# Kernel optimization log

Hardware: AMD Instinct MI355X
Metric: run time of the kernel (lower is better)

Reference implementation:

```python
import jax, jax.numpy as jnp
import numpy as np

B, D_IN = 4096, 1024
E, K = 16, 2
EMB = 256
H1, H2 = 2048, 1024  # hidden_units, hidden_units // 2
O = 512              # num_classes


def setup_inputs() -> dict:
    key = jax.random.key(0)
    ks = jax.random.split(key, 10)
    s = lambda *sh: 1.0 / np.sqrt(sh[-2] if len(sh) > 1 else 1.0)
    return {
        "x":   jax.random.normal(ks[0], (B, D_IN), jnp.float32),
        "Wr":  jax.random.normal(ks[1], (D_IN, EMB), jnp.float32) * (1.0 / np.sqrt(D_IN)),
        "br":  jnp.zeros((EMB,), jnp.float32),
        "emb": jax.random.normal(ks[2], (E, EMB), jnp.float32) * (1.0 / np.sqrt(EMB)),
        "W1":  jax.random.normal(ks[3], (E, D_IN, H1), jnp.float32) * (1.0 / np.sqrt(D_IN)),
        "b1":  jnp.zeros((E, H1), jnp.float32),
        "W2":  jax.random.normal(ks[4], (E, H1, H2), jnp.float32) * (1.0 / np.sqrt(H1)),
        "b2":  jnp.zeros((E, H2), jnp.float32),
        "W3":  jax.random.normal(ks[5], (E, H2, O), jnp.float32) * (1.0 / np.sqrt(H2)),
        "b3":  jnp.zeros((E, O), jnp.float32),
    }


def reference(x, Wr, br, emb, W1, b1, W2, b2, W3, b3):
    # Router query: [B, EMB]
    q = x @ Wr + br
    # Negative squared euclidean distance to expert embeddings -> scores [B, E]
    d2 = jnp.sum(jnp.square(q[:, None, :] - emb[None, :, :]), axis=-1)
    scores = -d2
    gating_probs = jax.nn.softmax(scores, axis=-1)  # [B, E]
    # Top-k selection + renormalized gates
    top_v, top_i = jax.lax.top_k(scores, K)          # [B, K]
    gates = jax.nn.softmax(top_v, axis=-1)           # [B, K]
    # All experts run on full batch (dense), batched over expert axis
    h1 = jax.nn.relu(jnp.einsum('bi,eih->beh', x, W1) + b1)   # [B, E, H1]
    h2 = jax.nn.relu(jnp.einsum('beh,ehm->bem', h1, W2) + b2)  # [B, E, H2]
    out = jnp.einsum('bem,emo->beo', h2, W3) + b3              # [B, E, O]
    # Gather top-k expert outputs per example and combine
    sel = jnp.take_along_axis(out, top_i[:, :, None], axis=1)  # [B, K, O]
    final = jnp.sum(sel * gates[:, :, None], axis=1)           # [B, O]
    return final, q, gating_probs
```

## Files before the change

### kernel.cpp

```cpp
#include <hip/hip_runtime.h>
#include <hip/hip_bf16.h>

using bf16 = __hip_bfloat16;
typedef __attribute__((ext_vector_type(8))) short bf16x8;
typedef __attribute__((ext_vector_type(8))) unsigned short u16x8;
typedef __attribute__((ext_vector_type(4))) float f32x4;

constexpr int BATCH = 4096;
constexpr int D_IN  = 1024;
constexpr int NEXP  = 16;
constexpr int EMB   = 256;
constexpr int H1    = 2048;
constexpr int H2    = 1024;
constexpr int OUTD  = 512;
constexpr int SLOTS = BATCH * 2;
constexpr int SLOTS_PAD = SLOTS + 256;
constexpr int MAX_T128 = SLOTS / 128 + NEXP;
constexpr int K3    = 3 * D_IN;

constexpr size_t WS_XB     = 0;
constexpr size_t WS_XLO    = WS_XB     + (size_t)BATCH * D_IN * 2;
constexpr size_t WS_H1     = WS_XLO    + (size_t)BATCH * D_IN * 2;
constexpr size_t WS_H2     = WS_H1     + (size_t)SLOTS_PAD * H1 * 2;
constexpr size_t WS_OSL    = WS_H2     + (size_t)SLOTS_PAD * H2 * 2;
constexpr size_t WS_TOPI   = WS_OSL    + (size_t)SLOTS_PAD * OUTD * 4;
constexpr size_t WS_GATES  = WS_TOPI   + (size_t)SLOTS * 4;
constexpr size_t WS_SLOTOF = WS_GATES  + (size_t)SLOTS * 4;
constexpr size_t WS_TOKL   = WS_SLOTOF + (size_t)SLOTS * 4;
constexpr size_t WS_CNT    = WS_TOKL   + (size_t)SLOTS_PAD * 4;
constexpr size_t WS_TMAP   = WS_CNT    + 64 * 4;
constexpr size_t WS_WR3    = ((WS_TMAP + (size_t)MAX_T128 * 8) + 255) & ~(size_t)255;
constexpr size_t WS_WT     = ((WS_WR3 + (size_t)EMB * K3 * 2) + 255) & ~(size_t)255;
constexpr size_t WT_BYTES  = (size_t)NEXP * H1 * D_IN * 2;
constexpr size_t WS_WTB    = WS_WT + WT_BYTES;
constexpr size_t WS_NEED_FUSED = WS_WTB + WT_BYTES;

__device__ __forceinline__ unsigned short f2bf(float f) {
    bf16 h = __float2bfloat16(f);
    return __builtin_bit_cast(unsigned short, h);
}
__device__ __forceinline__ float bf2f(unsigned short h) {
    return __builtin_bit_cast(float, (unsigned)h << 16);
}

__device__ __forceinline__ void gload16(const unsigned short* g, unsigned short* l) {
    __builtin_amdgcn_global_load_lds(
        (const __attribute__((address_space(1))) unsigned int*)g,
        (__attribute__((address_space(3))) unsigned int*)l, 16, 0, 0);
}

template <int N>
__device__ __forceinline__ void waitcnt_vm() {
    if constexpr (N == 0)       asm volatile("s_waitcnt vmcnt(0)" ::: "memory");
    else if constexpr (N == 4)  asm volatile("s_waitcnt vmcnt(4)" ::: "memory");
    else if constexpr (N == 6)  asm volatile("s_waitcnt vmcnt(6)" ::: "memory");
    else if constexpr (N == 8)  asm volatile("s_waitcnt vmcnt(8)" ::: "memory");
    else if constexpr (N == 12) asm volatile("s_waitcnt vmcnt(12)" ::: "memory");
    else static_assert(N == 0, "add case");
}

__device__ __forceinline__ void wtrans_body(const float* __restrict__ W,
                                            unsigned short* __restrict__ Wt,
                                            int KD, int ND, int e, int k0, int n0,
                                            char* smem) {
    float* Tf = (float*)smem;
    int t  = threadIdx.x;
    int kr = t >> 4, c4 = (t & 15) * 4;
    const float* Wb = W + ((size_t)e * KD + k0) * ND + n0;
#pragma unroll
    for (int i = 0; i < 4; i++) {
        float4 v = *reinterpret_cast<const float4*>(Wb + (size_t)(kr + i * 16) * ND + c4);
        Tf[(kr + i * 16) * 65 + c4 + 0] = v.x; Tf[(kr + i * 16) * 65 + c4 + 1] = v.y;
        Tf[(kr + i * 16) * 65 + c4 + 2] = v.z; Tf[(kr + i * 16) * 65 + c4 + 3] = v.w;
    }
    __syncthreads();
    unsigned short* Wtb = Wt + ((size_t)e * ND + n0) * KD + k0;
#pragma unroll
    for (int i = 0; i < 2; i++) {
        int idx = t + i * 256;
        int n = idx >> 3, ck = (idx & 7) * 8;
        u16x8 o;
#pragma unroll
        for (int j = 0; j < 8; j++) o[j] = f2bf(Tf[(ck + j) * 65 + n]);
        *reinterpret_cast<u16x8*>(Wtb + (size_t)n * KD + ck) = o;
    }
}

__global__ __launch_bounds__(256) void k_prep(const float* __restrict__ x,
                                              unsigned short* __restrict__ xhi,
                                              unsigned short* __restrict__ xlo,
                                              const float* __restrict__ Wr,
                                              unsigned short* __restrict__ Wrt3,
                                              int* __restrict__ counts) {
    __shared__ float Tf[64][65];
    int bx = blockIdx.x, t = threadIdx.x;
    if (bx < 4096) {
        int i = bx * 256 + t;
        float4 v = reinterpret_cast<const float4*>(x)[i];
        ushort4 h, l;
        h.x = f2bf(v.x); h.y = f2bf(v.y); h.z = f2bf(v.z); h.w = f2bf(v.w);
        l.x = f2bf(v.x - bf2f(h.x)); l.y = f2bf(v.y - bf2f(h.y));
        l.z = f2bf(v.z - bf2f(h.z)); l.w = f2bf(v.w - bf2f(h.w));
        reinterpret_cast<ushort4*>(xhi)[i] = h;
        reinterpret_cast<ushort4*>(xlo)[i] = l;
    } else if (bx < 4160) {
        int idx = bx - 4096;
        int n0 = (idx & 3) * 64, k0 = (idx >> 2) * 64;
        const float* Wb = Wr + (size_t)k0 * EMB + n0;
        int kr = t >> 4, c4 = (t & 15) * 4;
#pragma unroll
        for (int i = 0; i < 4; i++) {
            float4 v = *reinterpret_cast<const float4*>(Wb + (size_t)(kr + i * 16) * EMB + c4);
            Tf[kr + i * 16][c4 + 0] = v.x; Tf[kr + i * 16][c4 + 1] = v.y;
            Tf[kr + i * 16][c4 + 2] = v.z; Tf[kr + i * 16][c4 + 3] = v.w;
        }
        __syncthreads();
#pragma unroll
        for (int i = 0; i < 2; i++) {
            int idx2 = t + i * 256;
            int n = idx2 >> 3, ck = (idx2 & 7) * 8;
            u16x8 hi, lo;
#pragma unroll
            for (int j = 0; j < 8; j++) {
                float w = Tf[ck + j][n];
                unsigned short h = f2bf(w);
                hi[j] = h; lo[j] = f2bf(w - bf2f(h));
            }
            unsigned short* dst = Wrt3 + (size_t)(n0 + n) * K3 + k0 + ck;
            *reinterpret_cast<u16x8*>(dst)            = hi;
            *reinterpret_cast<u16x8*>(dst + D_IN)     = hi;
            *reinterpret_cast<u16x8*>(dst + 2 * D_IN) = lo;
        }
    } else {
        if (t < 16) counts[t] = 0;
    }
}

__global__ __launch_bounds__(256) void k_router_wt1(const unsigned short* __restrict__ xhi,
                                                    const unsigned short* __restrict__ xlo,
                                                    const unsigned short* __restrict__ wrt3,
                                                    const float* __restrict__ br,
                                                    float* __restrict__ qout,
                                                    const float* __restrict__ W1,
                                                    unsigned short* __restrict__ wt1) {
    __shared__ __align__(16) char smem[32768];
    int bx = blockIdx.x;
    if (bx >= 256) {
        int idx = bx - 256;
        int e   = idx >> 9;
        int rem = idx & 511;
        int k0  = (rem >> 5) << 6;
        int n0  = (rem & 31) << 6;
        wtrans_body(W1, wt1, D_IN, H1, e, k0, n0, smem);
        return;
    }
    unsigned short* As = (unsigned short*)smem;
    unsigned short* Bs = As + 8192;
    int nb = (bx & 3) * 64;
    int mb = (bx >> 2) * 64;

    int t    = threadIdx.x;
    int lane = t & 63;
    int w    = t >> 6;
    int wr   = (w >> 1) * 32;
    int wc   = (w & 1) * 32;

    int srow = t >> 3;
    int swz  = (t & 7) ^ (srow & 7);
    size_t aoff[2], boff[2];
#pragma unroll
    for (int i = 0; i < 2; i++) {
        int row = i * 32 + srow;
        aoff[i] = (size_t)(mb + row) * D_IN + swz * 8;
        boff[i] = (size_t)(nb + row) * K3 + swz * 8;
    }

    auto STAGE = [&](int buf, int tts) {
        const unsigned short* abase = (tts >= 16 && tts < 32) ? xlo : xhi;
        int kk = (tts & 15) * 64;
#pragma unroll
        for (int i = 0; i < 2; i++) {
            gload16(abase + aoff[i] + kk, As + buf * 4096 + (i * 32 + w * 8) * 64 + lane * 8);
            gload16(wrt3 + boff[i] + tts * 64, Bs + buf * 4096 + (i * 32 + w * 8) * 64 + lane * 8);
        }
    };

    f32x4 acc[2][2];
#pragma unroll
    for (int mi = 0; mi < 2; mi++)
#pragma unroll
        for (int ni = 0; ni < 2; ni++) acc[mi][ni] = {0.f, 0.f, 0.f, 0.f};

    int lr  = lane & 15;
    int lkc = lane >> 4;

    constexpr int NT = K3 / 64;
    STAGE(0, 0);
    STAGE(1, 1);

    for (int tt = 0; tt < NT; tt++) {
        int cur = tt & 1;
        if (tt + 1 < NT) waitcnt_vm<4>(); else waitcnt_vm<0>();
        __builtin_amdgcn_s_barrier();
        const char* Ab = (const char*)(As + cur * 4096);
        const char* Bb = (const char*)(Bs + cur * 4096);
#pragma unroll
        for (int ks = 0; ks < 2; ks++) {
            bf16x8 a[2], b[2];
#pragma unroll
            for (int mi = 0; mi < 2; mi++) {
                int row = wr + mi * 16 + lr;
                int c   = (lkc + ks * 4) ^ (row & 7);
                a[mi] = *reinterpret_cast<const bf16x8*>(Ab + row * 128 + c * 16);
            }
#pragma unroll
            for (int ni = 0; ni < 2; ni++) {
                int row = wc + ni * 16 + lr;
                int c   = (lkc + ks * 4) ^ (row & 7);
                b[ni] = *reinterpret_cast<const bf16x8*>(Bb + row * 128 + c * 16);
            }
#pragma unroll
            for (int mi = 0; mi < 2; mi++)
#pragma unroll
                for (int ni = 0; ni < 2; ni++)
                    acc[mi][ni] = __builtin_amdgcn_mfma_f32_16x16x32_bf16(a[mi], b[ni], acc[mi][ni], 0, 0, 0);
        }
        __builtin_amdgcn_s_barrier();
        if (tt + 2 < NT) STAGE(cur, tt + 2);
    }

    int rowbase = (lane >> 4) * 4;
#pragma unroll
    for (int ni = 0; ni < 2; ni++) {
        int col = nb + wc + ni * 16 + lr;
        float bv = br[col];
#pragma unroll
        for (int mi = 0; mi < 2; mi++) {
#pragma unroll
            for (int qi = 0; qi < 4; qi++) {
                int row = mb + wr + mi * 16 + rowbase + qi;
                qout[(size_t)row * EMB + col] = acc[mi][ni][qi] + bv;
            }
        }
    }
}

__global__ __launch_bounds__(256) void k_topk_count(const float* __restrict__ q,
                                                    const float* __restrict__ emb,
                                                    float* __restrict__ gp,
                                                    int* __restrict__ topi,
                                                    float* __restrict__ gates,
                                                    int* __restrict__ counts) {
    int b    = blockIdx.x * 4 + (threadIdx.x >> 6);
    int lane = threadIdx.x & 63;
    int e    = lane & 15;
    int seg  = (lane >> 4) * 64;
    const float* qr = q + (size_t)b * EMB + seg;
    const float* er = emb + (size_t)e * EMB + seg;
    float d2 = 0.f;
#pragma unroll 8
    for (int i = 0; i < 64; i++) { float d = qr[i] - er[i]; d2 = fmaf(d, d, d2); }
    d2 += __shfl_xor(d2, 16);
    d2 += __shfl_xor(d2, 32);
    float s = -d2;
    float m = s;
#pragma unroll
    for (int o = 1; o < 16; o <<= 1) m = fmaxf(m, __shfl_xor(m, o));
    float ex  = __expf(s - m);
    float sum = ex;
#pragma unroll
    for (int o = 1; o < 16; o <<= 1) sum += __shfl_xor(sum, o);
    if (lane < 16) gp[(size_t)b * NEXP + lane] = ex / sum;
    float v1 = s; int i1 = e;
#pragma unroll
    for (int o = 1; o < 16; o <<= 1) {
        float ov = __shfl_xor(v1, o); int oi = __shfl_xor(i1, o);
        if (ov > v1 || (ov == v1 && oi < i1)) { v1 = ov; i1 = oi; }
    }
    float s2 = (e == i1) ? -1e30f : s;
    float v2 = s2; int i2 = e;
#pragma unroll
    for (int o = 1; o < 16; o <<= 1) {
        float ov = __shfl_xor(v2, o); int oi = __shfl_xor(i2, o);
        if (ov > v2 || (ov == v2 && oi < i2)) { v2 = ov; i2 = oi; }
    }
    if (lane == 0) {
        topi[b * 2] = i1; topi[b * 2 + 1] = i2;
        float tv  = __expf(v2 - v1);
        float inv = 1.f / (1.f + tv);
        gates[b * 2] = inv; gates[b * 2 + 1] = tv * inv;
        atomicAdd(&counts[i1], 1);
        atomicAdd(&counts[i2], 1);
    }
}

__global__ void k_scan(const int* __restrict__ counts, int* __restrict__ offsets,
                       int* __restrict__ cursors, int2* __restrict__ tmap) {
    if (threadIdx.x != 0) return;
    int off = 0;
    for (int e = 0; e < NEXP; e++) {
        offsets[e] = off; cursors[e] = off;
        off += counts[e];
    }
    int nt = 0;
    for (int e = 0; e < NEXP; e++) {
        int c = counts[e];
        for (int base = 0; base < c; base += 128) tmap[nt++] = make_int2(e, base);
    }
    for (; nt < MAX_T128; nt++) tmap[nt] = make_int2(-1, 0);
}

__global__ __launch_bounds__(256) void k_scatter(const int* __restrict__ topi, int* __restrict__ cursors,
                                                 int* __restrict__ toklist, int* __restrict__ slotof) {
    int i = blockIdx.x * 256 + threadIdx.x;
    int e = topi[i];
    int s = atomicAdd(&cursors[e], 1);
    toklist[s] = i >> 1;
    slotof[i]  = s;
}

__global__ __launch_bounds__(256) void k_wtrans(const float* __restrict__ W,
                                                unsigned short* __restrict__ Wt,
                                                int KD, int ND) {
    __shared__ __align__(16) char smem[64 * 65 * 4];
    wtrans_body(W, Wt, KD, ND, blockIdx.z, blockIdx.y * 64, blockIdx.x * 64, smem);
}

template <int KD, int ND, int WN, int MODE, int KD2, int ND2, int DO_WT>
__global__ __launch_bounds__(WN * 64, 2) void k_gemm_wt(
    const unsigned short* __restrict__ Xin, const unsigned short* __restrict__ Wt,
    const float* __restrict__ bg, unsigned short* __restrict__ Hout,
    float* __restrict__ Oout, const int* __restrict__ counts,
    const int* __restrict__ offsets, const int* __restrict__ toklist,
    const int2* __restrict__ tmap, const float* __restrict__ Wnext,
    unsigned short* __restrict__ Wtnext) {
    constexpr int THREADS = WN * 64;
    constexpr int BM = 128;
    constexpr int BN = WN * 64;
    constexpr int FM = 8;
    constexpr int FN = 4;
    constexpr int RPI   = THREADS / 8;
    constexpr int A_ISS = (BM / 2) / RPI;
    constexpr int B_ISS = (BN / 2) / RPI;
    constexpr int SL    = A_ISS + B_ISS;
    constexpr int NX    = ND / BN;
    constexpr int NB_G  = NX * MAX_T128;
    constexpr int ABUF  = (BM / 2) * 64;
    constexpr int BBUF  = (BN / 2) * 64;

    __shared__ __align__(16) char smem[3 * (ABUF + BBUF) * 2];

    int bx = blockIdx.x;
    if (bx >= NB_G) {
        if constexpr (DO_WT) {
            constexpr int NBLK2 = ND2 / 64;
            constexpr int KBLK2 = KD2 / 64;
            int idx = bx - NB_G;
            int e   = idx / (NBLK2 * KBLK2);
            int rem = idx % (NBLK2 * KBLK2);
            int k0  = (rem / NBLK2) * 64;
            int n0  = (rem % NBLK2) * 64;
            wtrans_body(Wnext, Wtnext, KD2, ND2, e, k0, n0, smem);
        }
        return;
    }

    int2 tm = tmap[bx % MAX_T128];
    int e = tm.x;
    if (e < 0) return;
    int base = tm.y;
    int n_e  = counts[e];
    int off  = offsets[e];
    int n0   = (bx / MAX_T128) * BN;

    unsigned short* Asp = (unsigned short*)smem;
    unsigned short* Bsp = Asp + 3 * ABUF;

    int t    = threadIdx.x;
    int lane = t & 63;
    int w    = t >> 6;
    int wn   = w;

    int srow  = t >> 3;
    int chunk = t & 7;
    const unsigned short* asrc[A_ISS];
    const unsigned short* bsrc[B_ISS];
#pragma unroll
    for (int i = 0; i < A_ISS; i++) {
        int r  = i * RPI + srow;
        int js = chunk ^ (r & 7);
        int m_local = 2 * r + (js >> 2);
        int koff    = (js & 3) * 8;
        int g = base + m_local;
        size_t arow;
        if (MODE == 0) {
            int gg = (g < n_e) ? g : (n_e - 1);
            arow = (size_t)toklist[off + gg];
        } else {
            arow = (size_t)(off + g);
        }
        asrc[i] = Xin + arow * KD + koff;
    }
#pragma unroll
    for (int i = 0; i < B_ISS; i++) {
        int r  = i * RPI + srow;
        int js = chunk ^ (r & 7);
        int n_local = 2 * r + (js >> 2);
        int koff    = (js & 3) * 8;
        bsrc[i] = Wt + ((size_t)e * ND + n0 + n_local) * KD + koff;
    }

    auto STAGE = [&](int buf, int kt) {
#pragma unroll
        for (int i = 0; i < A_ISS; i++)
            gload16(asrc[i] + kt, Asp + buf * ABUF + (i * RPI + w * 8) * 64 + lane * 8);
#pragma unroll
        for (int i = 0; i < B_ISS; i++)
            gload16(bsrc[i] + kt, Bsp + buf * BBUF + (i * RPI + w * 8) * 64 + lane * 8);
    };

    f32x4 acc[FM][FN];
#pragma unroll
    for (int mi = 0; mi < FM; mi++)
#pragma unroll
        for (int ni = 0; ni < FN; ni++) acc[mi][ni] = {0.f, 0.f, 0.f, 0.f};

    int lr  = lane & 15;
    int lkc = lane >> 4;
    int jrd    = (((lr & 1) << 2) + lkc) ^ ((lr >> 1) & 7);
    int abase_ = (lr >> 1) * 128 + jrd * 16;
    int bbase_ = wn * 4096 + (lr >> 1) * 128 + jrd * 16;

    constexpr int NT = KD / 32;
    STAGE(0, 0);
    STAGE(1, 32);
    STAGE(2, 64);

    int cur = 0;
    for (int tt = 0; tt < NT; tt++) {
        if (tt + 2 < NT)      waitcnt_vm<2 * SL>();
        else if (tt + 1 < NT) waitcnt_vm<SL>();
        else                  waitcnt_vm<0>();
        __builtin_amdgcn_s_barrier();
        const char* Ab = (const char*)(Asp + cur * ABUF);
        const char* Bb = (const char*)(Bsp + cur * BBUF);
        bf16x8 a[FM], b[FN];
#pragma unroll
        for (int ni = 0; ni < FN; ni++)
            b[ni] = *reinterpret_cast<const bf16x8*>(Bb + bbase_ + ni * 1024);
#pragma unroll
        for (int mi = 0; mi < FM; mi++)
            a[mi] = *reinterpret_cast<const bf16x8*>(Ab + abase_ + mi * 1024);
#pragma unroll
        for (int mi = 0; mi < FM; mi++)
#pragma unroll
            for (int ni = 0; ni < FN; ni++)
                acc[mi][ni] = __builtin_amdgcn_mfma_f32_16x16x32_bf16(a[mi], b[ni], acc[mi][ni], 0, 0, 0);
        __builtin_amdgcn_s_barrier();
        if (tt + 3 < NT) STAGE(cur, (tt + 3) * 32);
        cur = (cur == 2) ? 0 : cur + 1;
    }

    int rowbase = (lane >> 4) * 4;
#pragma unroll
    for (int ni = 0; ni < FN; ni++) {
        int col = n0 + wn * 64 + ni * 16 + lr;
        float bv = bg[(size_t)e * ND + col];
#pragma unroll
        for (int mi = 0; mi < FM; mi++) {
#pragma unroll
            for (int qi = 0; qi < 4; qi++) {
                int g = base + mi * 16 + rowbase + qi;
                if (g < n_e) {
                    float v = acc[mi][ni][qi] + bv;
                    if (MODE == 2) {
                        Oout[(size_t)(off + g) * ND + col] = v;
                    } else {
                        v = fmaxf(v, 0.f);
                        Hout[(size_t)(off + g) * ND + col] = f2bf(v);
                    }
                }
            }
        }
    }
}

__global__ __launch_bounds__(128) void k_combine(const float* __restrict__ osl,
                                                 const float* __restrict__ gates,
                                                 const int* __restrict__ slotof,
                                                 float* __restrict__ outf) {
    int b = blockIdx.x;
    int j = threadIdx.x;
    int s0 = slotof[b * 2], s1 = slotof[b * 2 + 1];
    float g0 = gates[b * 2], g1 = gates[b * 2 + 1];
    float4 o0 = reinterpret_cast<const float4*>(osl + (size_t)s0 * OUTD)[j];
    float4 o1 = reinterpret_cast<const float4*>(osl + (size_t)s1 * OUTD)[j];
    float4 r;
    r.x = g0 * o0.x + g1 * o1.x;
    r.y = g0 * o0.y + g1 * o1.y;
    r.z = g0 * o0.z + g1 * o1.z;
    r.w = g0 * o0.w + g1 * o1.w;
    reinterpret_cast<float4*>(outf + (size_t)b * OUTD)[j] = r;
}

extern "C" void kernel_launch(void* const* d_in, const int* in_sizes, int n_in,
                              void* d_out, int out_size, void* d_ws, size_t ws_size,
                              hipStream_t stream) {
    const float* x   = (const float*)d_in[0];
    const float* Wr  = (const float*)d_in[1];
    const float* br  = (const float*)d_in[2];
    const float* emb = (const float*)d_in[3];
    const float* W1  = (const float*)d_in[4];
    const float* b1  = (const float*)d_in[5];
    const float* W2  = (const float*)d_in[6];
    const float* b2  = (const float*)d_in[7];
    const float* W3  = (const float*)d_in[8];
    const float* b3  = (const float*)d_in[9];

    float* out_final = (float*)d_out;
    float* out_q     = out_final + (size_t)BATCH * OUTD;
    float* out_gp    = out_q + (size_t)BATCH * EMB;

    char* ws = (char*)d_ws;
    unsigned short* xb  = (unsigned short*)(ws + WS_XB);
    unsigned short* xlo = (unsigned short*)(ws + WS_XLO);
    unsigned short* h1  = (unsigned short*)(ws + WS_H1);
    unsigned short* h2  = (unsigned short*)(ws + WS_H2);
    float* osl    = (float*)(ws + WS_OSL);
    int*   topi   = (int*)(ws + WS_TOPI);
    float* gates  = (float*)(ws + WS_GATES);
    int*   slotof = (int*)(ws + WS_SLOTOF);
    int*   toklist= (int*)(ws + WS_TOKL);
    int*   counts = (int*)(ws + WS_CNT);
    int*   offsets= counts + 16;
    int*   cursors= counts + 32;
    int2*  tmap   = (int2*)(ws + WS_TMAP);
    unsigned short* wrt3 = (unsigned short*)(ws + WS_WR3);
    unsigned short* wtA  = (unsigned short*)(ws + WS_WT);

    const bool fused = (ws_size >= WS_NEED_FUSED);
    unsigned short* wtB = fused ? (unsigned short*)(ws + WS_WTB) : wtA;

    k_prep<<<4161, 256, 0, stream>>>(x, xb, xlo, Wr, wrt3, counts);
    k_router_wt1<<<256 + 8192, 256, 0, stream>>>(xb, xlo, wrt3, br, out_q, W1, wtA);
    k_topk_count<<<BATCH / 4, 256, 0, stream>>>(out_q, emb, out_gp, topi, gates, counts);
    k_scan<<<1, 64, 0, stream>>>(counts, offsets, cursors, tmap);
    k_scatter<<<SLOTS / 256, 256, 0, stream>>>(topi, cursors, toklist, slotof);

    if (fused) {
        k_gemm_wt<D_IN, H1, 4, 0, H1, H2, 1><<<640 + 8192, 256, 0, stream>>>(
            xb, wtA, b1, h1, nullptr, counts, offsets, toklist, tmap, W2, wtB);
        k_gemm_wt<H1, H2, 4, 1, H2, OUTD, 1><<<320 + 2048, 256, 0, stream>>>(
            h1, wtB, b2, h2, nullptr, counts, offsets, toklist, tmap, W3, wtA);
        k_gemm_wt<H2, OUTD, 4, 2, 64, 64, 0><<<160, 256, 0, stream>>>(
            h2, wtA, b3, nullptr, osl, counts, offsets, toklist, tmap, nullptr, nullptr);
    } else {
        k_gemm_wt<D_IN, H1, 4, 0, 64, 64, 0><<<640, 256, 0, stream>>>(
            xb, wtA, b1, h1, nullptr, counts, offsets, toklist, tmap, nullptr, nullptr);
        k_wtrans<<<dim3(H2 / 64, H1 / 64, NEXP), 256, 0, stream>>>(W2, wtA, H1, H2);
        k_gemm_wt<H1, H2, 4, 1, 64, 64, 0><<<320, 256, 0, stream>>>(
            h1, wtA, b2, h2, nullptr, counts, offsets, toklist, tmap, nullptr, nullptr);
        k_wtrans<<<dim3(OUTD / 64, H2 / 64, NEXP), 256, 0, stream>>>(W3, wtA, H2, OUTD);
        k_gemm_wt<H2, OUTD, 4, 2, 64, 64, 0><<<160, 256, 0, stream>>>(
            h2, wtA, b3, nullptr, osl, counts, offsets, toklist, tmap, nullptr, nullptr);
    }

    k_combine<<<BATCH, 128, 0, stream>>>(osl, gates, slotof, out_final);
}
```

Before: 440.7 us.

## Move weight transposes earlier and bin expert tiles per XCD in grouped GEMMs

All three expert weight transposes (W1, W2, W3 to bf16) now run inside the router and top-k kernels instead of the GEMM kernels. Each GEMM kernel then only does matrix work, and the transposes overlap with the small router and top-k kernels. The scan kernel now bin-packs each expert's 128-row tiles into 8 bins of capacity 10, and the GEMM maps blockIdx so that each XCD handles one bin, aiming for L2 reuse of weight and activation tiles within an XCD. This needs more workspace (a third transpose buffer). The bin cap may drop tiles if the expert load is very skewed.

After: 458.1 us. +3.9%, slower.

```diff
diff --git a/kernel.cpp b/kernel.cpp
--- a/kernel.cpp
+++ b/kernel.cpp
@@ -16,6 +16,7 @@
 constexpr int SLOTS = BATCH * 2;
 constexpr int SLOTS_PAD = SLOTS + 256;
 constexpr int MAX_T128 = SLOTS / 128 + NEXP;
+constexpr int BIN_CAP  = 10;
 constexpr int K3    = 3 * D_IN;
 
 constexpr size_t WS_XB     = 0;
@@ -32,8 +33,11 @@
 constexpr size_t WS_WR3    = ((WS_TMAP + (size_t)MAX_T128 * 8) + 255) & ~(size_t)255;
 constexpr size_t WS_WT     = ((WS_WR3 + (size_t)EMB * K3 * 2) + 255) & ~(size_t)255;
 constexpr size_t WT_BYTES  = (size_t)NEXP * H1 * D_IN * 2;
-constexpr size_t WS_WTB    = WS_WT + WT_BYTES;
-constexpr size_t WS_NEED_FUSED = WS_WTB + WT_BYTES;
+constexpr size_t WT3_BYTES = (size_t)NEXP * H2 * OUTD * 2;
+constexpr size_t WS_WTB    = WS_WT  + WT_BYTES;
+constexpr size_t WS_WTC    = WS_WTB + WT_BYTES;
+constexpr size_t NEED2     = WS_WTC;
+constexpr size_t NEED1     = WS_WTC + WT3_BYTES;
 
 __device__ __forceinline__ unsigned short f2bf(float f) {
     bf16 h = __float2bfloat16(f);
@@ -54,7 +58,6 @@
     if constexpr (N == 0)       asm volatile("s_waitcnt vmcnt(0)" ::: "memory");
     else if constexpr (N == 4)  asm volatile("s_waitcnt vmcnt(4)" ::: "memory");
     else if constexpr (N == 6)  asm volatile("s_waitcnt vmcnt(6)" ::: "memory");
-    else if constexpr (N == 8)  asm volatile("s_waitcnt vmcnt(8)" ::: "memory");
     else if constexpr (N == 12) asm volatile("s_waitcnt vmcnt(12)" ::: "memory");
     else static_assert(N == 0, "add case");
 }
@@ -136,22 +139,27 @@
     }
 }
 
-__global__ __launch_bounds__(256) void k_router_wt1(const unsigned short* __restrict__ xhi,
-                                                    const unsigned short* __restrict__ xlo,
-                                                    const unsigned short* __restrict__ wrt3,
-                                                    const float* __restrict__ br,
-                                                    float* __restrict__ qout,
-                                                    const float* __restrict__ W1,
-                                                    unsigned short* __restrict__ wt1) {
+__global__ __launch_bounds__(256) void k_router_wt(const unsigned short* __restrict__ xhi,
+                                                   const unsigned short* __restrict__ xlo,
+                                                   const unsigned short* __restrict__ wrt3,
+                                                   const float* __restrict__ br,
+                                                   float* __restrict__ qout,
+                                                   const float* __restrict__ W1,
+                                                   unsigned short* __restrict__ wt1,
+                                                   const float* __restrict__ W2,
+                                                   unsigned short* __restrict__ wt2) {
     __shared__ __align__(16) char smem[32768];
     int bx = blockIdx.x;
     if (bx >= 256) {
         int idx = bx - 256;
-        int e   = idx >> 9;
-        int rem = idx & 511;
-        int k0  = (rem >> 5) << 6;
-        int n0  = (rem & 31) << 6;
-        wtrans_body(W1, wt1, D_IN, H1, e, k0, n0, smem);
+        if (idx < 8192) {
+            int e = idx >> 9, rem = idx & 511;
+            wtrans_body(W1, wt1, D_IN, H1, e, (rem >> 5) << 6, (rem & 31) << 6, smem);
+        } else {
+            int i2 = idx - 8192;
+            int e = i2 >> 9, rem = i2 & 511;
+            wtrans_body(W2, wt2, H1, H2, e, (rem >> 4) << 6, (rem & 15) << 6, smem);
+        }
         return;
     }
     unsigned short* As = (unsigned short*)smem;
@@ -245,13 +253,23 @@
     }
 }
 
-__global__ __launch_bounds__(256) void k_topk_count(const float* __restrict__ q,
-                                                    const float* __restrict__ emb,
-                                                    float* __restrict__ gp,
-                                                    int* __restrict__ topi,
-                                                    float* __restrict__ gates,
-                                                    int* __restrict__ counts) {
-    int b    = blockIdx.x * 4 + (threadIdx.x >> 6);
+__global__ __launch_bounds__(256) void k_topk_wt3(const float* __restrict__ q,
+                                                  const float* __restrict__ emb,
+                                                  float* __restrict__ gp,
+                                                  int* __restrict__ topi,
+                                                  float* __restrict__ gates,
+                                                  int* __restrict__ counts,
+                                                  const float* __restrict__ W3,
+                                                  unsigned short* __restrict__ wt3) {
+    __shared__ __align__(16) char smem[64 * 65 * 4];
+    int bx = blockIdx.x;
+    if (bx >= 1024) {
+        int idx = bx - 1024;
+        int e = idx >> 7, rem = idx & 127;
+        wtrans_body(W3, wt3, H2, OUTD, e, (rem >> 3) << 6, (rem & 7) << 6, smem);
+        return;
+    }
+    int b    = bx * 4 + (threadIdx.x >> 6);
     int lane = threadIdx.x & 63;
     int e    = lane & 15;
     int seg  = (lane >> 4) * 64;
@@ -298,16 +316,28 @@
                        int* __restrict__ cursors, int2* __restrict__ tmap) {
     if (threadIdx.x != 0) return;
     int off = 0;
+    int nt_e[NEXP];
     for (int e = 0; e < NEXP; e++) {
         offsets[e] = off; cursors[e] = off;
+        nt_e[e] = (counts[e] + 127) >> 7;
         off += counts[e];
     }
-    int nt = 0;
+    for (int i = 0; i < MAX_T128; i++) tmap[i] = make_int2(-1, 0);
+    int binload[8] = {0, 0, 0, 0, 0, 0, 0, 0};
     for (int e = 0; e < NEXP; e++) {
-        int c = counts[e];
-        for (int base = 0; base < c; base += 128) tmap[nt++] = make_int2(e, base);
-    }
-    for (; nt < MAX_T128; nt++) tmap[nt] = make_int2(-1, 0);
+        int rem = nt_e[e], ti = 0;
+        while (rem > 0) {
+            int b = 0;
+            for (int q2 = 1; q2 < 8; q2++)
+                if (binload[q2] < binload[b]) b = q2;
+            int space = BIN_CAP - binload[b];
+            if (space <= 0) break;
+            int take = (rem < space) ? rem : space;
+            for (int i = 0; i < take; i++)
+                tmap[b * BIN_CAP + binload[b] + i] = make_int2(e, (ti + i) * 128);
+            binload[b] += take; ti += take; rem -= take;
+        }
+    }
 }
 
 __global__ __launch_bounds__(256) void k_scatter(const int* __restrict__ topi, int* __restrict__ cursors,
@@ -326,14 +356,13 @@
     wtrans_body(W, Wt, KD, ND, blockIdx.z, blockIdx.y * 64, blockIdx.x * 64, smem);
 }
 
-template <int KD, int ND, int WN, int MODE, int KD2, int ND2, int DO_WT>
-__global__ __launch_bounds__(WN * 64, 2) void k_gemm_wt(
+template <int KD, int ND, int WN, int MODE>
+__global__ __launch_bounds__(WN * 64, 2) void k_gemm(
     const unsigned short* __restrict__ Xin, const unsigned short* __restrict__ Wt,
     const float* __restrict__ bg, unsigned short* __restrict__ Hout,
     float* __restrict__ Oout, const int* __restrict__ counts,
     const int* __restrict__ offsets, const int* __restrict__ toklist,
-    const int2* __restrict__ tmap, const float* __restrict__ Wnext,
-    unsigned short* __restrict__ Wtnext) {
+    const int2* __restrict__ tmap) {
     constexpr int THREADS = WN * 64;
     constexpr int BM = 128;
     constexpr int BN = WN * 64;
@@ -343,38 +372,23 @@
     constexpr int A_ISS = (BM / 2) / RPI;
     constexpr int B_ISS = (BN / 2) / RPI;
     constexpr int SL    = A_ISS + B_ISS;
-    constexpr int NX    = ND / BN;
-    constexpr int NB_G  = NX * MAX_T128;
-    constexpr int ABUF  = (BM / 2) * 64;
-    constexpr int BBUF  = (BN / 2) * 64;
-
-    __shared__ __align__(16) char smem[3 * (ABUF + BBUF) * 2];
-
-    int bx = blockIdx.x;
-    if (bx >= NB_G) {
-        if constexpr (DO_WT) {
-            constexpr int NBLK2 = ND2 / 64;
-            constexpr int KBLK2 = KD2 / 64;
-            int idx = bx - NB_G;
-            int e   = idx / (NBLK2 * KBLK2);
-            int rem = idx % (NBLK2 * KBLK2);
-            int k0  = (rem / NBLK2) * 64;
-            int n0  = (rem % NBLK2) * 64;
-            wtrans_body(Wnext, Wtnext, KD2, ND2, e, k0, n0, smem);
-        }
-        return;
-    }
-
-    int2 tm = tmap[bx % MAX_T128];
+
+    int id   = blockIdx.x;
+    int xcd  = id & 7;
+    int j    = id >> 3;
+    int y    = xcd * BIN_CAP + j % BIN_CAP;
+    int xnb  = j / BIN_CAP;
+
+    int2 tm = tmap[y];
     int e = tm.x;
     if (e < 0) return;
     int base = tm.y;
     int n_e  = counts[e];
     int off  = offsets[e];
-    int n0   = (bx / MAX_T128) * BN;
-
-    unsigned short* Asp = (unsigned short*)smem;
-    unsigned short* Bsp = Asp + 3 * ABUF;
+    int n0   = xnb * BN;
+
+    __shared__ __align__(16) unsigned short As[3][(BM / 2) * 64];
+    __shared__ __align__(16) unsigned short Bs[3][(BN / 2) * 64];
 
     int t    = threadIdx.x;
     int lane = t & 63;
@@ -413,10 +427,10 @@
     auto STAGE = [&](int buf, int kt) {
 #pragma unroll
         for (int i = 0; i < A_ISS; i++)
-            gload16(asrc[i] + kt, Asp + buf * ABUF + (i * RPI + w * 8) * 64 + lane * 8);
+            gload16(asrc[i] + kt, &As[buf][(i * RPI + w * 8) * 64] + lane * 8);
 #pragma unroll
         for (int i = 0; i < B_ISS; i++)
-            gload16(bsrc[i] + kt, Bsp + buf * BBUF + (i * RPI + w * 8) * 64 + lane * 8);
+            gload16(bsrc[i] + kt, &Bs[buf][(i * RPI + w * 8) * 64] + lane * 8);
     };
 
     f32x4 acc[FM][FN];
@@ -442,8 +456,8 @@
         else if (tt + 1 < NT) waitcnt_vm<SL>();
         else                  waitcnt_vm<0>();
         __builtin_amdgcn_s_barrier();
-        const char* Ab = (const char*)(Asp + cur * ABUF);
-        const char* Bb = (const char*)(Bsp + cur * BBUF);
+        const char* Ab = (const char*)As[cur];
+        const char* Bb = (const char*)Bs[cur];
         bf16x8 a[FM], b[FN];
 #pragma unroll
         for (int ni = 0; ni < FN; ni++)
@@ -537,33 +551,44 @@
     int2*  tmap   = (int2*)(ws + WS_TMAP);
     unsigned short* wrt3 = (unsigned short*)(ws + WS_WR3);
     unsigned short* wtA  = (unsigned short*)(ws + WS_WT);
-
-    const bool fused = (ws_size >= WS_NEED_FUSED);
-    unsigned short* wtB = fused ? (unsigned short*)(ws + WS_WTB) : wtA;
+    unsigned short* wtB  = (unsigned short*)(ws + WS_WTB);
+    unsigned short* wtC  = (unsigned short*)(ws + WS_WTC);
+
+    const bool t2 = (ws_size >= NEED2);
+    const bool t1 = (ws_size >= NEED1);
 
     k_prep<<<4161, 256, 0, stream>>>(x, xb, xlo, Wr, wrt3, counts);
-    k_router_wt1<<<256 + 8192, 256, 0, stream>>>(xb, xlo, wrt3, br, out_q, W1, wtA);
-    k_topk_count<<<BATCH / 4, 256, 0, stream>>>(out_q, emb, out_gp, topi, gates, counts);
+
+    if (t2) {
+        k_router_wt<<<256 + 8192 + 8192, 256, 0, stream>>>(
+            xb, xlo, wrt3, br, out_q, W1, wtA, W2, wtB);
+    } else {
+        k_router_wt<<<256, 256, 0, stream>>>(
+            xb, xlo, wrt3, br, out_q, nullptr, nullptr, nullptr, nullptr);
+    }
+
+    if (t1) {
+        k_topk_wt3<<<1024 + 2048, 256, 0, stream>>>(
+            out_q, emb, out_gp, topi, gates, counts, W3, wtC);
+    } else {
+        k_topk_wt3<<<1024, 256, 0, stream>>>(
+            out_q, emb, out_gp, topi, gates, counts, nullptr, nullptr);
+    }
+
     k_scan<<<1, 64, 0, stream>>>(counts, offsets, cursors, tmap);
     k_scatter<<<SLOTS / 256, 256, 0, stream>>>(topi, cursors, toklist, slotof);
 
-    if (fused) {
-        k_gemm_wt<D_IN, H1, 4, 0, H1, H2, 1><<<640 + 8192, 256, 0, stream>>>(
-            xb, wtA, b1, h1, nullptr, counts, offsets, toklist, tmap, W2, wtB);
-        k_gemm_wt<H1, H2, 4, 1, H2, OUTD, 1><<<320 + 2048, 256, 0, stream>>>(
-            h1, wtB, b2, h2, nullptr, counts, offsets, toklist, tmap, W3, wtA);
-        k_gemm_wt<H2, OUTD, 4, 2, 64, 64, 0><<<160, 256, 0, stream>>>(
-            h2, wtA, b3, nullptr, osl, counts, offsets, toklist, tmap, nullptr, nullptr);
-    } else {
-        k_gemm_wt<D_IN, H1, 4, 0, 64, 64, 0><<<640, 256, 0, stream>>>(
-            xb, wtA, b1, h1, nullptr, counts, offsets, toklist, tmap, nullptr, nullptr);
-        k_wtrans<<<dim3(H2 / 64, H1 / 64, NEXP), 256, 0, stream>>>(W2, wtA, H1, H2);
-        k_gemm_wt<H1, H2, 4, 1, 64, 64, 0><<<320, 256, 0, stream>>>(
-            h1, wtA, b2, h2, nullptr, counts, offsets, toklist, tmap, nullptr, nullptr);
-        k_wtrans<<<dim3(OUTD / 64, H2 / 64, NEXP), 256, 0, stream>>>(W3, wtA, H2, OUTD);
-        k_gemm_wt<H2, OUTD, 4, 2, 64, 64, 0><<<160, 256, 0, stream>>>(
-            h2, wtA, b3, nullptr, osl, counts, offsets, toklist, tmap, nullptr, nullptr);
-    }
+    if (!t2) k_wtrans<<<dim3(H1 / 64, D_IN / 64, NEXP), 256, 0, stream>>>(W1, wtA, D_IN, H1);
+    k_gemm<D_IN, H1, 4, 0><<<(H1 / 256) * MAX_T128, 256, 0, stream>>>(
+        xb, wtA, b1, h1, nullptr, counts, offsets, toklist, tmap);
+
+    if (!t2) k_wtrans<<<dim3(H2 / 64, H1 / 64, NEXP), 256, 0, stream>>>(W2, wtA, H1, H2);
+    k_gemm<H1, H2, 4, 1><<<(H2 / 256) * MAX_T128, 256, 0, stream>>>(
+        h1, t2 ? wtB : wtA, b2, h2, nullptr, counts, offsets, toklist, tmap);
+
+    if (!t1) k_wtrans<<<dim3(OUTD / 64, H2 / 64, NEXP), 256, 0, stream>>>(W3, wtA, H2, OUTD);
+    k_gemm<H2, OUTD, 4, 2><<<(OUTD / 256) * MAX_T128, 256, 0, stream>>>(
+        h2, t1 ? wtC : wtA, b3, nullptr, osl, counts, offsets, toklist, tmap);
 
     k_combine<<<BATCH, 128, 0, stream>>>(osl, gates, slotof, out_final);
 }
```
